# Kernel optimization log

Measured on AMD Instinct MI355X. Metric: run time of the kernel, lower is better.

Reference implementation:

```python
import jax, jax.numpy as jnp
import numpy as np

D_K = 64
SCALE = 1.0 / (D_K ** 0.5)
NEG_INF = float('-inf')


def setup_inputs() -> dict:
    key = jax.random.key(0)
    kq, kk, kv = jax.random.split(key, 3)
    B, H, S, D = 2, 16, 2048, D_K
    Q = jax.random.normal(kq, (B, H, S, D), dtype=jnp.float32)
    K = jax.random.normal(kk, (B, H, S, D), dtype=jnp.float32)
    V = jax.random.normal(kv, (B, H, S, D), dtype=jnp.float32)
    # causal mask: True = attend, False = masked (matches masked_fill(mask == False, -inf))
    mask = jnp.tril(jnp.ones((S, S), dtype=jnp.bool_))
    return {"Q": Q, "K": K, "V": V, "mask": mask}


def reference(Q, K, V, mask):
    # scores: [B, H, q, k]
    scores = jnp.einsum('bhqd,bhkd->bhqk', Q, K) * SCALE
    scores = jnp.where(mask, scores, NEG_INF)
    # hand-rolled stable softmax, same math as the torch module
    x_exp = jnp.exp(scores - jnp.max(scores, axis=-1, keepdims=True))
    attn = x_exp / jnp.sum(x_exp, axis=-1, keepdims=True)
    out = jnp.einsum('bhqk,bhkv->bhqv', attn, V)
    return out
```

## Files before the change

kernel.cpp:

```cpp
#include <hip/hip_runtime.h>
#include <hip/hip_bf16.h>

#define S_LEN   2048
#define D_DIM   64
#define BK      64
#define NBH     32

typedef __attribute__((ext_vector_type(8))) short  short8;
typedef __attribute__((ext_vector_type(4))) float  floatx4;

#define KLD   72
#define VTLD  72
#define PLD   72
#define OLD   65

#define VOFF  9216
#define POFF  18432
#define SMEM_BYTES 36864

__device__ __forceinline__ unsigned pk2(float lo, float hi) {
  __hip_bfloat162 h = __float22bfloat162_rn(float2{lo, hi});
  union { __hip_bfloat162 v; unsigned u; } c; c.v = h;
  return c.u;
}
__device__ __forceinline__ short8 pk8(const float* f) {
  union { short8 s; unsigned u[4]; } r;
  r.u[0] = pk2(f[0], f[1]); r.u[1] = pk2(f[2], f[3]);
  r.u[2] = pk2(f[4], f[5]); r.u[3] = pk2(f[6], f[7]);
  return r.s;
}
__device__ __forceinline__ float bf2f(unsigned short s) {
  union { unsigned u; float f; } c; c.u = ((unsigned)s) << 16; return c.f;
}

__global__ __launch_bounds__(256, 2)
void prep(const float* __restrict__ K, const float* __restrict__ V,
          unsigned short* __restrict__ Kbf, unsigned short* __restrict__ Vt)
{
  __shared__ unsigned short vt[64 * KLD];
  const int tid = threadIdx.x;
  const int bh  = blockIdx.x >> 5;
  const int k0  = (blockIdx.x & 31) * 64;

  {
    const int k   = k0 + (tid >> 2);
    const int seg = (tid & 3) * 16;
    const float* p = K + ((size_t)(bh * S_LEN + k)) * D_DIM + seg;
    union { float4 v[4]; float f[16]; } u;
    u.v[0] = *(const float4*)p;       u.v[1] = *(const float4*)(p + 4);
    u.v[2] = *(const float4*)(p + 8); u.v[3] = *(const float4*)(p + 12);
    unsigned short* dst = Kbf + ((size_t)(bh * S_LEN + k)) * D_DIM + seg;
    *(short8*)dst       = pk8(u.f);
    *(short8*)(dst + 8) = pk8(u.f + 8);
  }
  {
    const int kp2 = tid & 31;
    const int dg  = (tid >> 5) * 8;
    const float* p = V + ((size_t)(bh * S_LEN + k0 + 2 * kp2)) * D_DIM + dg;
    union { float4 v[2]; float f[8]; } x, y;
    x.v[0] = *(const float4*)p;            x.v[1] = *(const float4*)(p + 4);
    y.v[0] = *(const float4*)(p + D_DIM);  y.v[1] = *(const float4*)(p + D_DIM + 4);
#pragma unroll
    for (int i = 0; i < 8; ++i)
      *(unsigned*)&vt[(dg + i) * KLD + 2 * kp2] = pk2(x.f[i], y.f[i]);
  }
  __syncthreads();
  {
    const int d   = tid >> 2;
    const int seg = (tid & 3) * 16;
    short8 a = *(short8*)&vt[d * KLD + seg];
    short8 b = *(short8*)&vt[d * KLD + seg + 8];
    unsigned short* dst = Vt + ((size_t)(bh * D_DIM + d)) * S_LEN + k0 + seg;
    *(short8*)dst       = a;
    *(short8*)(dst + 8) = b;
  }
}

__global__ __launch_bounds__(256, 2)
void fa_fwd(const float* __restrict__ Qg,
            const unsigned short* __restrict__ Kbf,
            const unsigned short* __restrict__ Vt,
            float* __restrict__ Og,
            unsigned short* __restrict__ Opart,
            float* __restrict__ Lpart)
{
  __shared__ char smem[SMEM_BYTES];
  short* Klds  = (short*)smem;
  short* Vtlds = (short*)(smem + VOFF);

  const int tid  = threadIdx.x;
  const int wv   = tid >> 6;
  const int lane = tid & 63;
  const int col  = lane & 15;
  const int quad = lane >> 4;
  short* PA = (short*)(smem + POFF) + wv * (32 * PLD);
  short* PB = PA + 16 * PLD;
  float* Olds = (float*)smem + wv * (16 * OLD);

  int qi, bh, it0, itend, half = 0;
  bool split;
  if (blockIdx.x < 512) {
    split = true;
    qi    = 15 - ((int)blockIdx.x >> 6);
    bh    = ((int)blockIdx.x >> 1) & 31;
    half  = blockIdx.x & 1;
    const int nk = 2 * (qi + 1);
    const int h0 = nk >> 1;
    it0   = half ? h0 : 0;
    itend = half ? nk : h0;
  } else {
    split = false;
    const int u = blockIdx.x - 512;
    qi    = 7 - (u >> 5);
    bh    = u & 31;
    it0   = 0;
    itend = 2 * (qi + 1);
  }
  const int q0 = qi * 128;

  const float qscale = 0.18033688011112042f;
  const float*          Qb  = Qg  + (size_t)bh * S_LEN * D_DIM;
  const unsigned short* Kb  = Kbf + (size_t)bh * S_LEN * D_DIM;
  const unsigned short* Vtb = Vt  + (size_t)bh * D_DIM * S_LEN;
  float*                Ob  = Og  + (size_t)bh * S_LEN * D_DIM;

  const int srow = tid >> 2;
  const int sseg = (tid & 3) * 16;

  const int qws[2] = {q0 + wv * 16, q0 + 64 + wv * 16};

  short8 qf[2][2];
#pragma unroll
  for (int qt = 0; qt < 2; ++qt)
#pragma unroll
    for (int h = 0; h < 2; ++h) {
      const float* qp = Qb + (size_t)(qws[qt] + col) * D_DIM + h * 32 + quad * 8;
      union { float4 v[2]; float f[8]; } u;
      u.v[0] = *(const float4*)qp; u.v[1] = *(const float4*)(qp + 4);
      float t[8];
#pragma unroll
      for (int j = 0; j < 8; ++j) t[j] = u.f[j] * qscale;
      qf[qt][h] = pk8(t);
    }

  floatx4 o[2][4];
#pragma unroll
  for (int qt = 0; qt < 2; ++qt)
#pragma unroll
    for (int dt = 0; dt < 4; ++dt) o[qt][dt] = (floatx4){0.f,0.f,0.f,0.f};
  float l_run[2] = {0.f, 0.f};

  short8 kpre[2], vpre[2];
  {
    const unsigned short* kp = Kb  + (size_t)(it0 * BK + srow) * D_DIM + sseg;
    kpre[0] = *(const short8*)kp;  kpre[1] = *(const short8*)(kp + 8);
    const unsigned short* vp = Vtb + (size_t)srow * S_LEN + it0 * BK + sseg;
    vpre[0] = *(const short8*)vp;  vpre[1] = *(const short8*)(vp + 8);
  }

  for (int it = it0; it < itend; ++it) {
    __syncthreads();
    *(short8*)&Klds [srow * KLD  + sseg]     = kpre[0];
    *(short8*)&Klds [srow * KLD  + sseg + 8] = kpre[1];
    *(short8*)&Vtlds[srow * VTLD + sseg]     = vpre[0];
    *(short8*)&Vtlds[srow * VTLD + sseg + 8] = vpre[1];
    __syncthreads();

    if (it + 1 < itend) {
      const int kb2 = (it + 1) * BK;
      const unsigned short* kp = Kb  + (size_t)(kb2 + srow) * D_DIM + sseg;
      kpre[0] = *(const short8*)kp;  kpre[1] = *(const short8*)(kp + 8);
      const unsigned short* vp = Vtb + (size_t)srow * S_LEN + kb2 + sseg;
      vpre[0] = *(const short8*)vp;  vpre[1] = *(const short8*)(vp + 8);
    }

    const int  kb  = it * BK;
    const bool doA = (kb != q0 + 64);

    floatx4 st[2][4];
#pragma unroll
    for (int kt = 0; kt < 4; ++kt) {
      short8 kf0 = *(short8*)&Klds[(kt * 16 + col) * KLD + quad * 8];
      short8 kf1 = *(short8*)&Klds[(kt * 16 + col) * KLD + 32 + quad * 8];
      floatx4 c = (floatx4){0.f,0.f,0.f,0.f};
      c = __builtin_amdgcn_mfma_f32_16x16x32_bf16(kf0, qf[1][0], c, 0, 0, 0);
      c = __builtin_amdgcn_mfma_f32_16x16x32_bf16(kf1, qf[1][1], c, 0, 0, 0);
      st[1][kt] = c;
      if (doA) {
        floatx4 d = (floatx4){0.f,0.f,0.f,0.f};
        d = __builtin_amdgcn_mfma_f32_16x16x32_bf16(kf0, qf[0][0], d, 0, 0, 0);
        d = __builtin_amdgcn_mfma_f32_16x16x32_bf16(kf1, qf[0][1], d, 0, 0, 0);
        st[0][kt] = d;
      }
    }

    if (kb == q0) {
      const int qg = qws[0] + col;
#pragma unroll
      for (int kt = 0; kt < 4; ++kt)
#pragma unroll
        for (int r = 0; r < 4; ++r)
          if (kb + kt * 16 + quad * 4 + r > qg) st[0][kt][r] = -3.0e38f;
    }
    if (!doA) {
      const int qg = qws[1] + col;
#pragma unroll
      for (int kt = 0; kt < 4; ++kt)
#pragma unroll
        for (int r = 0; r < 4; ++r)
          if (kb + kt * 16 + quad * 4 + r > qg) st[1][kt][r] = -3.0e38f;
    }

#pragma unroll
    for (int qt = 0; qt < 2; ++qt) {
      if (qt == 0 && !doA) continue;
      float lsum = 0.f;
#pragma unroll
      for (int kt = 0; kt < 4; ++kt)
#pragma unroll
        for (int r = 0; r < 4; ++r) {
          const float p = __builtin_amdgcn_exp2f(st[qt][kt][r]);
          st[qt][kt][r] = p;
          lsum += p;
        }
      l_run[qt] += lsum;
      short* Pq = qt ? PB : PA;
#pragma unroll
      for (int kt = 0; kt < 4; ++kt) {
        uint2 w; w.x = pk2(st[qt][kt][0], st[qt][kt][1]); w.y = pk2(st[qt][kt][2], st[qt][kt][3]);
        *(uint2*)&Pq[col * PLD + kt * 16 + quad * 4] = w;
      }
    }

#pragma unroll
    for (int g = 0; g < 2; ++g) {
      short8 pfB = *(short8*)&PB[col * PLD + g * 32 + quad * 8];
      short8 pfA;
      if (doA) pfA = *(short8*)&PA[col * PLD + g * 32 + quad * 8];
#pragma unroll
      for (int dt = 0; dt < 4; ++dt) {
        short8 vf = *(short8*)&Vtlds[(dt * 16 + col) * VTLD + g * 32 + quad * 8];
        o[1][dt] = __builtin_amdgcn_mfma_f32_16x16x32_bf16(vf, pfB, o[1][dt], 0, 0, 0);
        if (doA)
          o[0][dt] = __builtin_amdgcn_mfma_f32_16x16x32_bf16(vf, pfA, o[0][dt], 0, 0, 0);
      }
    }
  }

  __syncthreads();
#pragma unroll
  for (int qt = 0; qt < 2; ++qt) {
    float l = l_run[qt];
    l += __shfl_xor(l, 16);
    l += __shfl_xor(l, 32);
    if (!split) {
      const float inv = 1.0f / l;
#pragma unroll
      for (int dt = 0; dt < 4; ++dt)
#pragma unroll
        for (int r = 0; r < 4; ++r)
          Olds[col * OLD + dt * 16 + quad * 4 + r] = o[qt][dt][r] * inv;
#pragma unroll
      for (int it2 = 0; it2 < 4; ++it2) {
        const int ql = it2 * 4 + quad;
        float4 w;
        w.x = Olds[ql * OLD + col * 4 + 0];
        w.y = Olds[ql * OLD + col * 4 + 1];
        w.z = Olds[ql * OLD + col * 4 + 2];
        w.w = Olds[ql * OLD + col * 4 + 3];
        *(float4*)(Ob + (size_t)(qws[qt] + ql) * D_DIM + col * 4) = w;
      }
    } else {
#pragma unroll
      for (int dt = 0; dt < 4; ++dt)
#pragma unroll
        for (int r = 0; r < 4; ++r)
          Olds[col * OLD + dt * 16 + quad * 4 + r] = o[qt][dt][r];
#pragma unroll
      for (int it2 = 0; it2 < 4; ++it2) {
        const int ql = it2 * 4 + quad;
        const int p  = qws[qt] + ql - 1024;
        float4 w;
        w.x = Olds[ql * OLD + col * 4 + 0];
        w.y = Olds[ql * OLD + col * 4 + 1];
        w.z = Olds[ql * OLD + col * 4 + 2];
        w.w = Olds[ql * OLD + col * 4 + 3];
        uint2 pw; pw.x = pk2(w.x, w.y); pw.y = pk2(w.z, w.w);
        *(uint2*)&Opart[((size_t)(half * 32 + bh) * 1024 + p) * 64 + col * 4] = pw;
      }
      if (quad == 0)
        Lpart[(half * 32 + bh) * 1024 + (qws[qt] + col - 1024)] = l;
    }
  }
}

__global__ __launch_bounds__(256, 2)
void merge(const unsigned short* __restrict__ Opart,
           const float* __restrict__ Lpart,
           float* __restrict__ Og)
{
  const int tid = threadIdx.x;
  const int gid = blockIdx.x * 64 + (tid >> 2);
  const int seg = (tid & 3) * 16;
  const int bh  = gid >> 10;
  const int p   = gid & 1023;
  const float la = Lpart[(0 * 32 + bh) * 1024 + p];
  const float lb = Lpart[(1 * 32 + bh) * 1024 + p];
  const float inv = 1.0f / (la + lb);
  const unsigned short* pa = Opart + ((size_t)(0 * 32 + bh) * 1024 + p) * 64 + seg;
  const unsigned short* pb = Opart + ((size_t)(1 * 32 + bh) * 1024 + p) * 64 + seg;
  union { short8 s; unsigned short h[8]; } a0, a1, b0, b1;
  a0.s = *(short8*)pa; a1.s = *(short8*)(pa + 8);
  b0.s = *(short8*)pb; b1.s = *(short8*)(pb + 8);
  float out[16];
#pragma unroll
  for (int j = 0; j < 8; ++j) out[j]     = (bf2f(a0.h[j]) + bf2f(b0.h[j])) * inv;
#pragma unroll
  for (int j = 0; j < 8; ++j) out[8 + j] = (bf2f(a1.h[j]) + bf2f(b1.h[j])) * inv;
  float* dst = Og + ((size_t)bh * S_LEN + 1024 + p) * D_DIM + seg;
#pragma unroll
  for (int j = 0; j < 4; ++j)
    *(float4*)(dst + 4 * j) = *(float4*)&out[4 * j];
}

extern "C" void kernel_launch(void* const* d_in, const int* in_sizes, int n_in,
                              void* d_out, int out_size, void* d_ws, size_t ws_size,
                              hipStream_t stream) {
  const float* Q = (const float*)d_in[0];
  const float* K = (const float*)d_in[1];
  const float* V = (const float*)d_in[2];
  float* O = (float*)d_out;
  unsigned short* Kbf   = (unsigned short*)d_ws;
  unsigned short* Vt    = Kbf + (size_t)NBH * S_LEN * D_DIM;
  unsigned short* Opart = Vt  + (size_t)NBH * S_LEN * D_DIM;
  float*          Lpart = (float*)(Opart + (size_t)2 * 32 * 1024 * 64);

  hipLaunchKernelGGL(prep,   dim3(NBH * (S_LEN / 64)), dim3(256), 0, stream, K, V, Kbf, Vt);
  hipLaunchKernelGGL(fa_fwd, dim3(768), dim3(256), 0, stream, Q, Kbf, Vt, O, Opart, Lpart);
  hipLaunchKernelGGL(merge,  dim3(512), dim3(256), 0, stream, Opart, Lpart, O);
}
```

Before: 143.1 us.

## Fuse K/V bf16 conversion and V transpose into attention kernel, drop prep pass

Removes the separate prep kernel that converted K to bf16 and wrote a transposed bf16 V to workspace. The attention kernel now loads fp32 K and V directly, packs them to bf16 and transposes V while storing into LDS each iteration. This saves one launch and a full read/write round trip of K and V through global memory. In exchange the main loop reads twice as many bytes per tile, and K/V tiles are re-converted by every query block, which adds ALU work and register pressure.

New measurement: 144.6 us. Within noise of the previous version (+1.0%).

```diff
diff --git a/kernel.cpp b/kernel.cpp
--- a/kernel.cpp
+++ b/kernel.cpp
@@ -34,52 +34,9 @@
 }
 
 __global__ __launch_bounds__(256, 2)
-void prep(const float* __restrict__ K, const float* __restrict__ V,
-          unsigned short* __restrict__ Kbf, unsigned short* __restrict__ Vt)
-{
-  __shared__ unsigned short vt[64 * KLD];
-  const int tid = threadIdx.x;
-  const int bh  = blockIdx.x >> 5;
-  const int k0  = (blockIdx.x & 31) * 64;
-
-  {
-    const int k   = k0 + (tid >> 2);
-    const int seg = (tid & 3) * 16;
-    const float* p = K + ((size_t)(bh * S_LEN + k)) * D_DIM + seg;
-    union { float4 v[4]; float f[16]; } u;
-    u.v[0] = *(const float4*)p;       u.v[1] = *(const float4*)(p + 4);
-    u.v[2] = *(const float4*)(p + 8); u.v[3] = *(const float4*)(p + 12);
-    unsigned short* dst = Kbf + ((size_t)(bh * S_LEN + k)) * D_DIM + seg;
-    *(short8*)dst       = pk8(u.f);
-    *(short8*)(dst + 8) = pk8(u.f + 8);
-  }
-  {
-    const int kp2 = tid & 31;
-    const int dg  = (tid >> 5) * 8;
-    const float* p = V + ((size_t)(bh * S_LEN + k0 + 2 * kp2)) * D_DIM + dg;
-    union { float4 v[2]; float f[8]; } x, y;
-    x.v[0] = *(const float4*)p;            x.v[1] = *(const float4*)(p + 4);
-    y.v[0] = *(const float4*)(p + D_DIM);  y.v[1] = *(const float4*)(p + D_DIM + 4);
-#pragma unroll
-    for (int i = 0; i < 8; ++i)
-      *(unsigned*)&vt[(dg + i) * KLD + 2 * kp2] = pk2(x.f[i], y.f[i]);
-  }
-  __syncthreads();
-  {
-    const int d   = tid >> 2;
-    const int seg = (tid & 3) * 16;
-    short8 a = *(short8*)&vt[d * KLD + seg];
-    short8 b = *(short8*)&vt[d * KLD + seg + 8];
-    unsigned short* dst = Vt + ((size_t)(bh * D_DIM + d)) * S_LEN + k0 + seg;
-    *(short8*)dst       = a;
-    *(short8*)(dst + 8) = b;
-  }
-}
-
-__global__ __launch_bounds__(256, 2)
 void fa_fwd(const float* __restrict__ Qg,
-            const unsigned short* __restrict__ Kbf,
-            const unsigned short* __restrict__ Vt,
+            const float* __restrict__ Kg,
+            const float* __restrict__ Vg,
             float* __restrict__ Og,
             unsigned short* __restrict__ Opart,
             float* __restrict__ Lpart)
@@ -119,13 +76,15 @@
   const int q0 = qi * 128;
 
   const float qscale = 0.18033688011112042f;
-  const float*          Qb  = Qg  + (size_t)bh * S_LEN * D_DIM;
-  const unsigned short* Kb  = Kbf + (size_t)bh * S_LEN * D_DIM;
-  const unsigned short* Vtb = Vt  + (size_t)bh * D_DIM * S_LEN;
-  float*                Ob  = Og  + (size_t)bh * S_LEN * D_DIM;
+  const float* Qb = Qg + (size_t)bh * S_LEN * D_DIM;
+  const float* Kb = Kg + (size_t)bh * S_LEN * D_DIM;
+  const float* Vb = Vg + (size_t)bh * S_LEN * D_DIM;
+  float*       Ob = Og + (size_t)bh * S_LEN * D_DIM;
 
   const int srow = tid >> 2;
   const int sseg = (tid & 3) * 16;
+  const int kp2  = tid & 31;
+  const int dg   = (tid >> 5) * 8;
 
   const int qws[2] = {q0 + wv * 16, q0 + 64 + wv * 16};
 
@@ -150,28 +109,34 @@
     for (int dt = 0; dt < 4; ++dt) o[qt][dt] = (floatx4){0.f,0.f,0.f,0.f};
   float l_run[2] = {0.f, 0.f};
 
-  short8 kpre[2], vpre[2];
+  union f16u { float4 v[4]; float f[16]; };
+  f16u kpre, vpre;
   {
-    const unsigned short* kp = Kb  + (size_t)(it0 * BK + srow) * D_DIM + sseg;
-    kpre[0] = *(const short8*)kp;  kpre[1] = *(const short8*)(kp + 8);
-    const unsigned short* vp = Vtb + (size_t)srow * S_LEN + it0 * BK + sseg;
-    vpre[0] = *(const short8*)vp;  vpre[1] = *(const short8*)(vp + 8);
+    const float* kp = Kb + (size_t)(it0 * BK + srow) * D_DIM + sseg;
+    kpre.v[0] = *(const float4*)kp;       kpre.v[1] = *(const float4*)(kp + 4);
+    kpre.v[2] = *(const float4*)(kp + 8); kpre.v[3] = *(const float4*)(kp + 12);
+    const float* vp = Vb + (size_t)(it0 * BK + 2 * kp2) * D_DIM + dg;
+    vpre.v[0] = *(const float4*)vp;             vpre.v[1] = *(const float4*)(vp + 4);
+    vpre.v[2] = *(const float4*)(vp + D_DIM);   vpre.v[3] = *(const float4*)(vp + D_DIM + 4);
   }
 
   for (int it = it0; it < itend; ++it) {
     __syncthreads();
-    *(short8*)&Klds [srow * KLD  + sseg]     = kpre[0];
-    *(short8*)&Klds [srow * KLD  + sseg + 8] = kpre[1];
-    *(short8*)&Vtlds[srow * VTLD + sseg]     = vpre[0];
-    *(short8*)&Vtlds[srow * VTLD + sseg + 8] = vpre[1];
+    *(short8*)&Klds[srow * KLD + sseg]     = pk8(kpre.f);
+    *(short8*)&Klds[srow * KLD + sseg + 8] = pk8(kpre.f + 8);
+#pragma unroll
+    for (int i = 0; i < 8; ++i)
+      *(unsigned*)&Vtlds[(dg + i) * VTLD + 2 * kp2] = pk2(vpre.f[i], vpre.f[8 + i]);
     __syncthreads();
 
     if (it + 1 < itend) {
       const int kb2 = (it + 1) * BK;
-      const unsigned short* kp = Kb  + (size_t)(kb2 + srow) * D_DIM + sseg;
-      kpre[0] = *(const short8*)kp;  kpre[1] = *(const short8*)(kp + 8);
-      const unsigned short* vp = Vtb + (size_t)srow * S_LEN + kb2 + sseg;
-      vpre[0] = *(const short8*)vp;  vpre[1] = *(const short8*)(vp + 8);
+      const float* kp = Kb + (size_t)(kb2 + srow) * D_DIM + sseg;
+      kpre.v[0] = *(const float4*)kp;       kpre.v[1] = *(const float4*)(kp + 4);
+      kpre.v[2] = *(const float4*)(kp + 8); kpre.v[3] = *(const float4*)(kp + 12);
+      const float* vp = Vb + (size_t)(kb2 + 2 * kp2) * D_DIM + dg;
+      vpre.v[0] = *(const float4*)vp;             vpre.v[1] = *(const float4*)(vp + 4);
+      vpre.v[2] = *(const float4*)(vp + D_DIM);   vpre.v[3] = *(const float4*)(vp + D_DIM + 4);
     }
 
     const int  kb  = it * BK;
@@ -330,12 +295,9 @@
   const float* K = (const float*)d_in[1];
   const float* V = (const float*)d_in[2];
   float* O = (float*)d_out;
-  unsigned short* Kbf   = (unsigned short*)d_ws;
-  unsigned short* Vt    = Kbf + (size_t)NBH * S_LEN * D_DIM;
-  unsigned short* Opart = Vt  + (size_t)NBH * S_LEN * D_DIM;
+  unsigned short* Opart = (unsigned short*)d_ws;
   float*          Lpart = (float*)(Opart + (size_t)2 * 32 * 1024 * 64);
 
-  hipLaunchKernelGGL(prep,   dim3(NBH * (S_LEN / 64)), dim3(256), 0, stream, K, V, Kbf, Vt);
-  hipLaunchKernelGGL(fa_fwd, dim3(768), dim3(256), 0, stream, Q, Kbf, Vt, O, Opart, Lpart);
+  hipLaunchKernelGGL(fa_fwd, dim3(768), dim3(256), 0, stream, Q, K, V, O, Opart, Lpart);
   hipLaunchKernelGGL(merge,  dim3(512), dim3(256), 0, stream, Opart, Lpart, O);
 }
```
